# Kernel optimization log

Hardware: AMD Instinct MI355X
Metric: run time of the kernel (lower is better)

Reference implementation:

```python
import jax, jax.numpy as jnp
import numpy as np

THETA = 0.5


def setup_inputs() -> dict:
    key = jax.random.key(0)
    k1, k2, k3 = jax.random.split(key, 3)
    B, S, D = 64, 4096, 256
    # strictly increasing times with small positive deltas
    dt = jax.random.uniform(k1, (B, S, 1), dtype=jnp.float32) * 0.01 + 1e-4
    t = jnp.cumsum(dt, axis=-2)
    x0 = jax.random.normal(k2, (B, 1, D), dtype=jnp.float32)
    z = jax.random.normal(k3, (B, S, D), dtype=jnp.float32)
    return {"t": t, "x0": x0, "z": z}


def reference(t, x0, z):
    # t: [B,S,1], x0: [B,1,D], z: [B,S,D]
    # OU recurrence: x_i = c_i * x_{i-1} + sqrt(1 - c_i^2) * z_i,  c_i = exp(-theta * dt_i)
    delta = jnp.diff(t, axis=-2, prepend=jnp.zeros_like(t[..., :1, :]))  # [B,S,1]
    c = jnp.exp(-THETA * delta)                                          # [B,S,1]
    b = jnp.sqrt(1.0 - c * c) * z                                        # [B,S,D]
    # fold initial state into step 0: b_0 += c_0 * x0
    b = b.at[..., 0, :].add(c[..., 0, :] * x0[..., 0, :])
    a = jnp.broadcast_to(c, b.shape)                                     # [B,S,D]

    def combine(e1, e2):
        a1, b1 = e1
        a2, b2 = e2
        return (a2 * a1, a2 * b1 + b2)

    _, x = jax.lax.associative_scan(combine, (a, b), axis=-2)
    return x  # [B,S,D]
```

## Files before the change

kernel.cpp:

```cpp
#include <hip/hip_runtime.h>


#define THETA 0.5f
constexpr int Bn = 64;
constexpr int Sn = 4096;
constexpr int Dn = 256;
constexpr int CHUNK = 64;
constexpr int NC = Sn / CHUNK;

__global__ __launch_bounds__(64) void k_agg(
    const float* __restrict__ t,
    const float* __restrict__ x0,
    const float* __restrict__ z,
    float* __restrict__ agg)
{
    const int blk = blockIdx.x;
    const int b = blk / NC;
    const int k = blk % NC;
    const int lane = threadIdx.x;
    const int s0 = k * CHUNK;

    __shared__ float cs[CHUNK];
    __shared__ float ss[CHUNK];
    {
        const int r = s0 + lane;
        float tcur = t[b * Sn + r];
        float tprev = (r == 0) ? 0.0f : t[b * Sn + r - 1];
        float c = __expf(-THETA * (tcur - tprev));
        cs[lane] = c;
        ss[lane] = sqrtf(fmaxf(0.0f, 1.0f - c * c));
    }
    __syncthreads();

    const int d0 = lane * 4;
    float a0 = 0.f, a1 = 0.f, a2 = 0.f, a3 = 0.f;
    if (k == 0) {
        const float4 xv = *(const float4*)(x0 + (size_t)b * Dn + d0);
        a0 = xv.x; a1 = xv.y; a2 = xv.z; a3 = xv.w;
    }

    const float* zp = z + ((size_t)b * Sn + s0) * Dn + d0;
#pragma unroll 4
    for (int r = 0; r < CHUNK; ++r) {
        const float4 zv = *(const float4*)zp;
        zp += Dn;
        const float c = cs[r];
        const float sv = ss[r];
        a0 = fmaf(c, a0, sv * zv.x);
        a1 = fmaf(c, a1, sv * zv.y);
        a2 = fmaf(c, a2, sv * zv.z);
        a3 = fmaf(c, a3, sv * zv.w);
    }

    float4* ap = (float4*)(agg + ((size_t)b * NC + k) * Dn + d0);
    *ap = make_float4(a0, a1, a2, a3);
}

__global__ __launch_bounds__(256) void k_scan(
    const float* __restrict__ t,
    float* __restrict__ agg)
{
    const int b = blockIdx.x;
    const int d = threadIdx.x;

    __shared__ float As[NC];
    if (d < NC) {
        const int k = d;
        float tend = t[b * Sn + k * CHUNK + CHUNK - 1];
        float tpe = (k == 0) ? 0.0f : t[b * Sn + k * CHUNK - 1];
        As[k] = __expf(-THETA * (tend - tpe));
    }
    __syncthreads();

    float cin = 0.0f;
    float* ap = agg + (size_t)b * NC * Dn + d;
#pragma unroll 8
    for (int k = 0; k < NC; ++k) {
        const float bk = ap[(size_t)k * Dn];
        ap[(size_t)k * Dn] = cin;
        cin = fmaf(As[k], cin, bk);
    }
}

__global__ __launch_bounds__(64) void k_final(
    const float* __restrict__ t,
    const float* __restrict__ x0,
    const float* __restrict__ z,
    const float* __restrict__ carry,
    float* __restrict__ out)
{
    const int blk = blockIdx.x;
    const int b = blk / NC;
    const int k = blk % NC;
    const int lane = threadIdx.x;
    const int s0 = k * CHUNK;

    __shared__ float cs[CHUNK];
    __shared__ float ss[CHUNK];
    {
        const int r = s0 + lane;
        float tcur = t[b * Sn + r];
        float tprev = (r == 0) ? 0.0f : t[b * Sn + r - 1];
        float c = __expf(-THETA * (tcur - tprev));
        cs[lane] = c;
        ss[lane] = sqrtf(fmaxf(0.0f, 1.0f - c * c));
    }
    __syncthreads();

    const int d0 = lane * 4;
    float a0, a1, a2, a3;
    if (k == 0) {
        const float4 xv = *(const float4*)(x0 + (size_t)b * Dn + d0);
        a0 = xv.x; a1 = xv.y; a2 = xv.z; a3 = xv.w;
    } else {
        const float4 cv = *(const float4*)(carry + ((size_t)b * NC + k) * Dn + d0);
        a0 = cv.x; a1 = cv.y; a2 = cv.z; a3 = cv.w;
    }

    const float* zp = z + ((size_t)b * Sn + s0) * Dn + d0;
    float* op = out + ((size_t)b * Sn + s0) * Dn + d0;
#pragma unroll 4
    for (int r = 0; r < CHUNK; ++r) {
        const float4 zv = *(const float4*)zp;
        zp += Dn;
        const float c = cs[r];
        const float sv = ss[r];
        a0 = fmaf(c, a0, sv * zv.x);
        a1 = fmaf(c, a1, sv * zv.y);
        a2 = fmaf(c, a2, sv * zv.z);
        a3 = fmaf(c, a3, sv * zv.w);
        *(float4*)op = make_float4(a0, a1, a2, a3);
        op += Dn;
    }
}

extern "C" void kernel_launch(void* const* d_in, const int* in_sizes, int n_in,
                              void* d_out, int out_size, void* d_ws, size_t ws_size,
                              hipStream_t stream) {
    const float* t  = (const float*)d_in[0];
    const float* x0 = (const float*)d_in[1];
    const float* z  = (const float*)d_in[2];
    float* out = (float*)d_out;

    float* agg = (float*)d_ws;

    k_agg<<<Bn * NC, 64, 0, stream>>>(t, x0, z, agg);
    k_scan<<<Bn, 256, 0, stream>>>(t, agg);
    k_final<<<Bn * NC, 64, 0, stream>>>(t, x0, z, agg, out);
}
```

Measured before the change: 501.5 us.

## Prefetch z rows in registers, pack four chunks per block, nontemporal final I/O

Every kernel now keeps an eight-deep register ring of upcoming z (or agg) rows so several loads are in flight while the serial FMA chain runs. k_agg and k_final put four 64-lane waves, one chunk each, in a 256-thread block. k_scan is split into four column tiles per batch to run more blocks. k_final uses nontemporal loads and stores for the streamed z and output. The change trades more register pressure and a fully unrolled loop for more memory-level parallelism on this bandwidth-bound recurrence.

```diff
diff --git a/kernel.cpp b/kernel.cpp
--- a/kernel.cpp
+++ b/kernel.cpp
@@ -7,130 +7,146 @@
 constexpr int Dn = 256;
 constexpr int CHUNK = 64;
 constexpr int NC = Sn / CHUNK;
+constexpr int WPB = 4;
+constexpr int NCB = NC / WPB;
+constexpr int PF = 8;
 
-__global__ __launch_bounds__(64) void k_agg(
+typedef float f32x4 __attribute__((ext_vector_type(4)));
+
+__global__ __launch_bounds__(256) void k_agg(
     const float* __restrict__ t,
     const float* __restrict__ x0,
     const float* __restrict__ z,
     float* __restrict__ agg)
 {
-    const int blk = blockIdx.x;
-    const int b = blk / NC;
-    const int k = blk % NC;
-    const int lane = threadIdx.x;
-    const int s0 = k * CHUNK;
+    const int w    = threadIdx.x >> 6;
+    const int lane = threadIdx.x & 63;
+    const int b    = blockIdx.x / NCB;
+    const int k    = (blockIdx.x % NCB) * WPB + w;
+    const int s0   = k * CHUNK;
 
-    __shared__ float cs[CHUNK];
-    __shared__ float ss[CHUNK];
+    __shared__ float2 css[WPB][CHUNK];
     {
         const int r = s0 + lane;
-        float tcur = t[b * Sn + r];
-        float tprev = (r == 0) ? 0.0f : t[b * Sn + r - 1];
-        float c = __expf(-THETA * (tcur - tprev));
-        cs[lane] = c;
-        ss[lane] = sqrtf(fmaxf(0.0f, 1.0f - c * c));
+        const float tcur  = t[b * Sn + r];
+        const float tprev = (r == 0) ? 0.0f : t[b * Sn + r - 1];
+        const float c = __expf(-THETA * (tcur - tprev));
+        css[w][lane] = make_float2(c, sqrtf(fmaxf(0.0f, 1.0f - c * c)));
     }
     __syncthreads();
 
     const int d0 = lane * 4;
     float a0 = 0.f, a1 = 0.f, a2 = 0.f, a3 = 0.f;
     if (k == 0) {
-        const float4 xv = *(const float4*)(x0 + (size_t)b * Dn + d0);
+        const f32x4 xv = *(const f32x4*)(x0 + (size_t)b * Dn + d0);
         a0 = xv.x; a1 = xv.y; a2 = xv.z; a3 = xv.w;
     }
 
     const float* zp = z + ((size_t)b * Sn + s0) * Dn + d0;
-#pragma unroll 4
+    f32x4 buf[PF];
+#pragma unroll
+    for (int i = 0; i < PF; ++i)
+        buf[i] = *(const f32x4*)(zp + (size_t)i * Dn);
+#pragma unroll
     for (int r = 0; r < CHUNK; ++r) {
-        const float4 zv = *(const float4*)zp;
-        zp += Dn;
-        const float c = cs[r];
-        const float sv = ss[r];
-        a0 = fmaf(c, a0, sv * zv.x);
-        a1 = fmaf(c, a1, sv * zv.y);
-        a2 = fmaf(c, a2, sv * zv.z);
-        a3 = fmaf(c, a3, sv * zv.w);
+        const f32x4 zv = buf[r & (PF - 1)];
+        if (r + PF < CHUNK)
+            buf[r & (PF - 1)] = *(const f32x4*)(zp + (size_t)(r + PF) * Dn);
+        const float2 cv = css[w][r];
+        a0 = fmaf(cv.x, a0, cv.y * zv.x);
+        a1 = fmaf(cv.x, a1, cv.y * zv.y);
+        a2 = fmaf(cv.x, a2, cv.y * zv.z);
+        a3 = fmaf(cv.x, a3, cv.y * zv.w);
     }
 
-    float4* ap = (float4*)(agg + ((size_t)b * NC + k) * Dn + d0);
-    *ap = make_float4(a0, a1, a2, a3);
+    f32x4 av; av.x = a0; av.y = a1; av.z = a2; av.w = a3;
+    *(f32x4*)(agg + ((size_t)b * NC + k) * Dn + d0) = av;
 }
 
-__global__ __launch_bounds__(256) void k_scan(
+__global__ __launch_bounds__(64) void k_scan(
     const float* __restrict__ t,
     float* __restrict__ agg)
 {
-    const int b = blockIdx.x;
-    const int d = threadIdx.x;
+    const int b    = blockIdx.x >> 2;
+    const int tile = blockIdx.x & 3;
+    const int lane = threadIdx.x;
+    const int d    = tile * 64 + lane;
 
     __shared__ float As[NC];
-    if (d < NC) {
-        const int k = d;
-        float tend = t[b * Sn + k * CHUNK + CHUNK - 1];
-        float tpe = (k == 0) ? 0.0f : t[b * Sn + k * CHUNK - 1];
-        As[k] = __expf(-THETA * (tend - tpe));
+    {
+        const float tend = t[b * Sn + lane * CHUNK + CHUNK - 1];
+        const float tpe  = (lane == 0) ? 0.0f : t[b * Sn + lane * CHUNK - 1];
+        As[lane] = __expf(-THETA * (tend - tpe));
     }
     __syncthreads();
 
+    float* ap = agg + (size_t)b * NC * Dn + d;
     float cin = 0.0f;
-    float* ap = agg + (size_t)b * NC * Dn + d;
-#pragma unroll 8
+    float buf[PF];
+#pragma unroll
+    for (int i = 0; i < PF; ++i) buf[i] = ap[(size_t)i * Dn];
+#pragma unroll
     for (int k = 0; k < NC; ++k) {
-        const float bk = ap[(size_t)k * Dn];
+        const float bk = buf[k & (PF - 1)];
+        if (k + PF < NC) buf[k & (PF - 1)] = ap[(size_t)(k + PF) * Dn];
         ap[(size_t)k * Dn] = cin;
         cin = fmaf(As[k], cin, bk);
     }
 }
 
-__global__ __launch_bounds__(64) void k_final(
+__global__ __launch_bounds__(256) void k_final(
     const float* __restrict__ t,
     const float* __restrict__ x0,
     const float* __restrict__ z,
     const float* __restrict__ carry,
     float* __restrict__ out)
 {
-    const int blk = blockIdx.x;
-    const int b = blk / NC;
-    const int k = blk % NC;
-    const int lane = threadIdx.x;
-    const int s0 = k * CHUNK;
+    const int w    = threadIdx.x >> 6;
+    const int lane = threadIdx.x & 63;
+    const int b    = blockIdx.x / NCB;
+    const int k    = (blockIdx.x % NCB) * WPB + w;
+    const int s0   = k * CHUNK;
 
-    __shared__ float cs[CHUNK];
-    __shared__ float ss[CHUNK];
+    __shared__ float2 css[WPB][CHUNK];
     {
         const int r = s0 + lane;
-        float tcur = t[b * Sn + r];
-        float tprev = (r == 0) ? 0.0f : t[b * Sn + r - 1];
-        float c = __expf(-THETA * (tcur - tprev));
-        cs[lane] = c;
-        ss[lane] = sqrtf(fmaxf(0.0f, 1.0f - c * c));
+        const float tcur  = t[b * Sn + r];
+        const float tprev = (r == 0) ? 0.0f : t[b * Sn + r - 1];
+        const float c = __expf(-THETA * (tcur - tprev));
+        css[w][lane] = make_float2(c, sqrtf(fmaxf(0.0f, 1.0f - c * c)));
     }
     __syncthreads();
 
     const int d0 = lane * 4;
     float a0, a1, a2, a3;
     if (k == 0) {
-        const float4 xv = *(const float4*)(x0 + (size_t)b * Dn + d0);
+        const f32x4 xv = *(const f32x4*)(x0 + (size_t)b * Dn + d0);
         a0 = xv.x; a1 = xv.y; a2 = xv.z; a3 = xv.w;
     } else {
-        const float4 cv = *(const float4*)(carry + ((size_t)b * NC + k) * Dn + d0);
+        const f32x4 cv = *(const f32x4*)(carry + ((size_t)b * NC + k) * Dn + d0);
         a0 = cv.x; a1 = cv.y; a2 = cv.z; a3 = cv.w;
     }
 
     const float* zp = z + ((size_t)b * Sn + s0) * Dn + d0;
     float* op = out + ((size_t)b * Sn + s0) * Dn + d0;
-#pragma unroll 4
+
+    f32x4 buf[PF];
+#pragma unroll
+    for (int i = 0; i < PF; ++i)
+        buf[i] = __builtin_nontemporal_load((const f32x4*)(zp + (size_t)i * Dn));
+#pragma unroll
     for (int r = 0; r < CHUNK; ++r) {
-        const float4 zv = *(const float4*)zp;
-        zp += Dn;
-        const float c = cs[r];
-        const float sv = ss[r];
-        a0 = fmaf(c, a0, sv * zv.x);
-        a1 = fmaf(c, a1, sv * zv.y);
-        a2 = fmaf(c, a2, sv * zv.z);
-        a3 = fmaf(c, a3, sv * zv.w);
-        *(float4*)op = make_float4(a0, a1, a2, a3);
-        op += Dn;
+        const f32x4 zv = buf[r & (PF - 1)];
+        if (r + PF < CHUNK)
+            buf[r & (PF - 1)] =
+                __builtin_nontemporal_load((const f32x4*)(zp + (size_t)(r + PF) * Dn));
+        const float2 cv = css[w][r];
+        a0 = fmaf(cv.x, a0, cv.y * zv.x);
+        a1 = fmaf(cv.x, a1, cv.y * zv.y);
+        a2 = fmaf(cv.x, a2, cv.y * zv.z);
+        a3 = fmaf(cv.x, a3, cv.y * zv.w);
+        f32x4 ov; ov.x = a0; ov.y = a1; ov.z = a2; ov.w = a3;
+        __builtin_nontemporal_store(ov, (f32x4*)(op + (size_t)r * Dn));
     }
 }
 
@@ -144,7 +160,7 @@
 
     float* agg = (float*)d_ws;
 
-    k_agg<<<Bn * NC, 64, 0, stream>>>(t, x0, z, agg);
-    k_scan<<<Bn, 256, 0, stream>>>(t, agg);
-    k_final<<<Bn * NC, 64, 0, stream>>>(t, x0, z, agg, out);
+    k_agg  <<<Bn * NCB, 256, 0, stream>>>(t, x0, z, agg);
+    k_scan <<<Bn * 4,    64, 0, stream>>>(t, agg);
+    k_final<<<Bn * NCB, 256, 0, stream>>>(t, x0, z, agg, out);
 }
```

Measured after the change: 482.4 us. 1.04x faster.

## Fuse three-pass chunked scan into single-pass decoupled look-back kernel

Applied to the files above, without the earlier changes.

Replaces the aggregate/scan/final three-kernel pipeline with one persistent kernel that takes chunks by atomic ticket, holds each 128-row chunk of z in registers, publishes chunk aggregates and inclusive prefixes with flags, and resolves the carry through decoupled look-back. z is read from global memory once instead of twice, and the inter-kernel launches and the serial per-batch scan pass go away. The cost is 128 floats of register storage per thread, spin-waiting on flags, and a memset before each launch.

```diff
diff --git a/kernel.cpp b/kernel.cpp
--- a/kernel.cpp
+++ b/kernel.cpp
@@ -5,132 +5,116 @@
 constexpr int Bn = 64;
 constexpr int Sn = 4096;
 constexpr int Dn = 256;
-constexpr int CHUNK = 64;
-constexpr int NC = Sn / CHUNK;
+constexpr int CHUNK = 128;
+constexpr int NC   = Sn / CHUNK;
+constexpr int NTICK = Bn * NC;
+constexpr int NBLK = 512;
 
-__global__ __launch_bounds__(64) void k_agg(
+__global__ __launch_bounds__(256, 2) void k_ou(
     const float* __restrict__ t,
     const float* __restrict__ x0,
     const float* __restrict__ z,
-    float* __restrict__ agg)
+    float* __restrict__ out,
+    float* __restrict__ agg,
+    float* __restrict__ inc,
+    unsigned* __restrict__ flags,
+    unsigned* __restrict__ ticket)
 {
-    const int blk = blockIdx.x;
-    const int b = blk / NC;
-    const int k = blk % NC;
-    const int lane = threadIdx.x;
-    const int s0 = k * CHUNK;
+    const int d = threadIdx.x;
+    __shared__ float cs[CHUNK], ss[CHUNK], Ps[CHUNK];
+    __shared__ float As[NC];
+    __shared__ unsigned tks;
 
-    __shared__ float cs[CHUNK];
-    __shared__ float ss[CHUNK];
-    {
-        const int r = s0 + lane;
-        float tcur = t[b * Sn + r];
-        float tprev = (r == 0) ? 0.0f : t[b * Sn + r - 1];
-        float c = __expf(-THETA * (tcur - tprev));
-        cs[lane] = c;
-        ss[lane] = sqrtf(fmaxf(0.0f, 1.0f - c * c));
-    }
-    __syncthreads();
+    for (;;) {
+        __syncthreads();
+        if (d == 0)
+            tks = __hip_atomic_fetch_add(ticket, 1u, __ATOMIC_RELAXED,
+                                         __HIP_MEMORY_SCOPE_AGENT);
+        __syncthreads();
+        const unsigned T = tks;
+        if (T >= NTICK) return;
+        const int b  = (int)(T / NC);
+        const int k  = (int)(T % NC);
+        const int s0 = k * CHUNK;
+        const float* tb = t + (size_t)b * Sn;
 
-    const int d0 = lane * 4;
-    float a0 = 0.f, a1 = 0.f, a2 = 0.f, a3 = 0.f;
-    if (k == 0) {
-        const float4 xv = *(const float4*)(x0 + (size_t)b * Dn + d0);
-        a0 = xv.x; a1 = xv.y; a2 = xv.z; a3 = xv.w;
-    }
+        if (d < CHUNK) {
+            const int r = d;
+            const float tc   = tb[s0 + r];
+            const float tp   = (s0 + r == 0) ? 0.0f : tb[s0 + r - 1];
+            const float tpre = (s0 == 0) ? 0.0f : tb[s0 - 1];
+            const float c = __expf(-THETA * (tc - tp));
+            cs[r] = c;
+            ss[r] = sqrtf(fmaxf(0.0f, 1.0f - c * c));
+            Ps[r] = __expf(-THETA * (tc - tpre));
+        } else if (d < CHUNK + NC) {
+            const int j = d - CHUNK;
+            const float te = tb[j * CHUNK + CHUNK - 1];
+            const float tp = (j == 0) ? 0.0f : tb[j * CHUNK - 1];
+            As[j] = __expf(-THETA * (te - tp));
+        }
+        __syncthreads();
 
-    const float* zp = z + ((size_t)b * Sn + s0) * Dn + d0;
-#pragma unroll 4
-    for (int r = 0; r < CHUNK; ++r) {
-        const float4 zv = *(const float4*)zp;
-        zp += Dn;
-        const float c = cs[r];
-        const float sv = ss[r];
-        a0 = fmaf(c, a0, sv * zv.x);
-        a1 = fmaf(c, a1, sv * zv.y);
-        a2 = fmaf(c, a2, sv * zv.z);
-        a3 = fmaf(c, a3, sv * zv.w);
-    }
+        const float* zp = z + ((size_t)b * Sn + s0) * Dn + d;
+        float v[CHUNK];
+#pragma unroll
+        for (int r = 0; r < CHUNK; ++r)
+            v[r] = __builtin_nontemporal_load(zp + (size_t)r * Dn);
+        float a = 0.0f;
+#pragma unroll
+        for (int r = 0; r < CHUNK; ++r) {
+            a = fmaf(cs[r], a, ss[r] * v[r]);
+            v[r] = a;
+        }
 
-    float4* ap = (float4*)(agg + ((size_t)b * NC + k) * Dn + d0);
-    *ap = make_float4(a0, a1, a2, a3);
-}
+        float E;
+        if (k == 0) {
+            E = x0[(size_t)b * Dn + d];
+        } else {
+            __hip_atomic_store(agg + (size_t)T * Dn + d, a,
+                               __ATOMIC_RELAXED, __HIP_MEMORY_SCOPE_AGENT);
+            __threadfence();
+            __syncthreads();
+            if (d == 0)
+                __hip_atomic_store(&flags[T], 1u, __ATOMIC_RELEASE,
+                                   __HIP_MEMORY_SCOPE_AGENT);
+            E = 0.0f;
+            float Amul = 1.0f;
+            int j = k - 1;
+            for (;;) {
+                unsigned f;
+                do {
+                    f = __hip_atomic_load(&flags[(size_t)b * NC + j],
+                                          __ATOMIC_ACQUIRE,
+                                          __HIP_MEMORY_SCOPE_AGENT);
+                    f = __builtin_amdgcn_readfirstlane(f);
+                    if (f == 0u) __builtin_amdgcn_s_sleep(2);
+                } while (f == 0u);
+                const float* pj = ((f == 2u) ? inc : agg)
+                                  + ((size_t)b * NC + j) * Dn + d;
+                const float val = __hip_atomic_load(pj, __ATOMIC_RELAXED,
+                                                    __HIP_MEMORY_SCOPE_AGENT);
+                E = fmaf(Amul, val, E);
+                if (f == 2u) break;
+                Amul *= As[j];
+                --j;
+            }
+        }
 
-__global__ __launch_bounds__(256) void k_scan(
-    const float* __restrict__ t,
-    float* __restrict__ agg)
-{
-    const int b = blockIdx.x;
-    const int d = threadIdx.x;
+        const float myinc = fmaf(As[k], E, a);
+        __hip_atomic_store(inc + (size_t)T * Dn + d, myinc,
+                           __ATOMIC_RELAXED, __HIP_MEMORY_SCOPE_AGENT);
+        __threadfence();
+        __syncthreads();
+        if (d == 0)
+            __hip_atomic_store(&flags[T], 2u, __ATOMIC_RELEASE,
+                               __HIP_MEMORY_SCOPE_AGENT);
 
-    __shared__ float As[NC];
-    if (d < NC) {
-        const int k = d;
-        float tend = t[b * Sn + k * CHUNK + CHUNK - 1];
-        float tpe = (k == 0) ? 0.0f : t[b * Sn + k * CHUNK - 1];
-        As[k] = __expf(-THETA * (tend - tpe));
-    }
-    __syncthreads();
-
-    float cin = 0.0f;
-    float* ap = agg + (size_t)b * NC * Dn + d;
-#pragma unroll 8
-    for (int k = 0; k < NC; ++k) {
-        const float bk = ap[(size_t)k * Dn];
-        ap[(size_t)k * Dn] = cin;
-        cin = fmaf(As[k], cin, bk);
-    }
-}
-
-__global__ __launch_bounds__(64) void k_final(
-    const float* __restrict__ t,
-    const float* __restrict__ x0,
-    const float* __restrict__ z,
-    const float* __restrict__ carry,
-    float* __restrict__ out)
-{
-    const int blk = blockIdx.x;
-    const int b = blk / NC;
-    const int k = blk % NC;
-    const int lane = threadIdx.x;
-    const int s0 = k * CHUNK;
-
-    __shared__ float cs[CHUNK];
-    __shared__ float ss[CHUNK];
-    {
-        const int r = s0 + lane;
-        float tcur = t[b * Sn + r];
-        float tprev = (r == 0) ? 0.0f : t[b * Sn + r - 1];
-        float c = __expf(-THETA * (tcur - tprev));
-        cs[lane] = c;
-        ss[lane] = sqrtf(fmaxf(0.0f, 1.0f - c * c));
-    }
-    __syncthreads();
-
-    const int d0 = lane * 4;
-    float a0, a1, a2, a3;
-    if (k == 0) {
-        const float4 xv = *(const float4*)(x0 + (size_t)b * Dn + d0);
-        a0 = xv.x; a1 = xv.y; a2 = xv.z; a3 = xv.w;
-    } else {
-        const float4 cv = *(const float4*)(carry + ((size_t)b * NC + k) * Dn + d0);
-        a0 = cv.x; a1 = cv.y; a2 = cv.z; a3 = cv.w;
-    }
-
-    const float* zp = z + ((size_t)b * Sn + s0) * Dn + d0;
-    float* op = out + ((size_t)b * Sn + s0) * Dn + d0;
-#pragma unroll 4
-    for (int r = 0; r < CHUNK; ++r) {
-        const float4 zv = *(const float4*)zp;
-        zp += Dn;
-        const float c = cs[r];
-        const float sv = ss[r];
-        a0 = fmaf(c, a0, sv * zv.x);
-        a1 = fmaf(c, a1, sv * zv.y);
-        a2 = fmaf(c, a2, sv * zv.z);
-        a3 = fmaf(c, a3, sv * zv.w);
-        *(float4*)op = make_float4(a0, a1, a2, a3);
-        op += Dn;
+        float* op = out + ((size_t)b * Sn + s0) * Dn + d;
+#pragma unroll
+        for (int r = 0; r < CHUNK; ++r)
+            __builtin_nontemporal_store(fmaf(Ps[r], E, v[r]),
+                                        op + (size_t)r * Dn);
     }
 }
 
@@ -142,9 +126,11 @@
     const float* z  = (const float*)d_in[2];
     float* out = (float*)d_out;
 
-    float* agg = (float*)d_ws;
+    float*    agg    = (float*)d_ws;
+    float*    inc    = agg + (size_t)NTICK * Dn;
+    unsigned* flags  = (unsigned*)(inc + (size_t)NTICK * Dn);
+    unsigned* ticket = flags + NTICK;
 
-    k_agg<<<Bn * NC, 64, 0, stream>>>(t, x0, z, agg);
-    k_scan<<<Bn, 256, 0, stream>>>(t, agg);
-    k_final<<<Bn * NC, 64, 0, stream>>>(t, x0, z, agg, out);
+    hipMemsetAsync(flags, 0, (NTICK + 1) * sizeof(unsigned), stream);
+    k_ou<<<NBLK, 256, 0, stream>>>(t, x0, z, out, agg, inc, flags, ticket);
 }
```

Result: slower. 1.572 ms (+213.4%).
